# Performance work log

Hardware: AMD Instinct MI355X
Metric: run time of the kernel (lower is better)

Reference implementation:

```python
import jax, jax.numpy as jnp
import numpy as np

NUM_HEADS = 16

def setup_inputs() -> dict:
    key = jax.random.key(0)
    ks = jax.random.split(key, 8)
    T, S, B, E = 2048, 2048, 4, 1024
    s = 0.02
    return {
        "query": jax.random.normal(ks[0], (T, B, E), jnp.float32),
        "key": jax.random.normal(ks[1], (S, B, E), jnp.float32),
        "value": jax.random.normal(ks[2], (S, B, E), jnp.float32),
        "q_proj_weight": jax.random.normal(ks[3], (E, E), jnp.float32) * s,
        "k_proj_weight": jax.random.normal(ks[4], (E, E), jnp.float32) * s,
        "v_proj_weight": jax.random.normal(ks[5], (E, E), jnp.float32) * s,
        "out_proj_weight": jax.random.normal(ks[6], (E, E), jnp.float32) * s,
        "out_proj_bias": jax.random.normal(ks[7], (E,), jnp.float32) * s,
    }

def reference(query, key, value, q_proj_weight, k_proj_weight, v_proj_weight,
              out_proj_weight, out_proj_bias):
    T, B, E = query.shape
    S = key.shape[0]
    H = NUM_HEADS
    hd = E // H
    # F.linear: x @ W.T
    q = jnp.einsum('tbe,fe->tbf', query, q_proj_weight) * (float(hd) ** -0.5)
    k = jnp.einsum('sbe,fe->sbf', key, k_proj_weight)
    v = jnp.einsum('sbe,fe->sbf', value, v_proj_weight)
    # [len, B, E] -> [B*H, len, hd]  (view then transpose, as in torch)
    q = q.reshape(T, B * H, hd).transpose(1, 0, 2)
    k = k.reshape(S, B * H, hd).transpose(1, 0, 2)
    v = v.reshape(S, B * H, hd).transpose(1, 0, 2)
    scores = jnp.einsum('nth,nsh->nts', q, k)      # [B*H, T, S]
    attn = jax.nn.softmax(scores, axis=-1)          # dropout p=0.0 -> identity
    out = jnp.einsum('nts,nsh->nth', attn, v)       # [B*H, T, hd]
    out = out.transpose(1, 0, 2).reshape(T, B, E)
    attn_output = jnp.einsum('tbe,fe->tbf', out, out_proj_weight) + out_proj_bias
    # faithful to original: view(num_heads, batch, T, S) of the [B*H,T,S] buffer
    avg_weights = attn.reshape(H, B, T, S).sum(axis=0) / H  # [B, T, S]
    return attn_output, avg_weights
```

## Files before the change

kernel.cpp:

```cpp
#include <hip/hip_runtime.h>
#include <stdint.h>

#define T_LEN 2048
#define S_LEN 2048
#define BATCH 4
#define EMB 1024
#define NH 16
#define HD 64
#define MROWS 8192

typedef __attribute__((ext_vector_type(8))) __bf16 bfx8;
typedef __attribute__((ext_vector_type(4))) float fx4;
typedef __attribute__((ext_vector_type(16))) float fx16;
typedef __attribute__((ext_vector_type(8))) unsigned short usx8;
typedef __attribute__((ext_vector_type(2))) unsigned int ux2;
typedef __attribute__((ext_vector_type(4))) unsigned int ux4;

typedef __attribute__((address_space(1))) const void GV;
typedef __attribute__((address_space(3))) void LV;
#define GLL(gp, lp) __builtin_amdgcn_global_load_lds((GV*)(gp), (LV*)(lp), 16, 0, 0)

#define QSCALE 0.18033688011112042591f
#define M0F 12.0f

static __device__ __forceinline__ unsigned short f2bf(float f) {
  unsigned int u = __float_as_uint(f);
  u += 0x7fffu + ((u >> 16) & 1u);
  return (unsigned short)(u >> 16);
}

static __device__ __forceinline__ unsigned int cvt_pk(float lo, float hi) {
  unsigned int r;
  asm("v_cvt_pk_bf16_f32 %0, %1, %2" : "=v"(r) : "v"(lo), "v"(hi));
  return r;
}

static __device__ __forceinline__ void plswap(unsigned int &a, unsigned int &b) {
  auto r = __builtin_amdgcn_permlane32_swap((int)a, (int)b, false, false);
  a = (unsigned int)r[0];
  b = (unsigned int)r[1];
}

#define PIPE_BARRIER(N)                                              \
  do {                                                               \
    asm volatile("s_waitcnt vmcnt(" #N ")" ::: "memory");            \
    __builtin_amdgcn_s_barrier();                                    \
    asm volatile("" ::: "memory");                                   \
  } while (0)

__global__ __launch_bounds__(256) void cast_all(
    const float* __restrict__ q, const float* __restrict__ k, const float* __restrict__ v,
    const float* __restrict__ wq, const float* __restrict__ wk, const float* __restrict__ wv,
    const float* __restrict__ wo,
    unsigned short* __restrict__ xq, unsigned short* __restrict__ xk, unsigned short* __restrict__ xv,
    unsigned short* __restrict__ bwq, unsigned short* __restrict__ bwk, unsigned short* __restrict__ bwv,
    unsigned short* __restrict__ bwo)
{
  const long IN8 = (long)MROWS * EMB / 8;
  const long W8  = (long)EMB * EMB / 8;
  const long total = 3 * IN8 + 4 * W8;
  for (long i = (long)blockIdx.x * 256 + threadIdx.x; i < total; i += (long)gridDim.x * 256) {
    const float* s; unsigned short* d; long off;
    if (i < 3 * IN8) {
      long wch = i / IN8; off = i - wch * IN8;
      s = (wch == 0) ? q : (wch == 1) ? k : v;
      d = (wch == 0) ? xq : (wch == 1) ? xk : xv;
    } else {
      long j = i - 3 * IN8; long wch = j / W8; off = j - wch * W8;
      s = (wch == 0) ? wq : (wch == 1) ? wk : (wch == 2) ? wv : wo;
      d = (wch == 0) ? bwq : (wch == 1) ? bwk : (wch == 2) ? bwv : bwo;
    }
    const float4* sp = (const float4*)(s + off * 8);
    float4 a = sp[0], b2 = sp[1];
    usx8 r;
    r[0] = f2bf(a.x);  r[1] = f2bf(a.y);  r[2] = f2bf(a.z);  r[3] = f2bf(a.w);
    r[4] = f2bf(b2.x); r[5] = f2bf(b2.y); r[6] = f2bf(b2.z); r[7] = f2bf(b2.w);
    *(usx8*)(d + off * 8) = r;
  }
}

template<int EPI>
__global__ __launch_bounds__(256) void gemm_bt(
    const unsigned short* __restrict__ A,
    const unsigned short* __restrict__ Bw,
    void* __restrict__ Cp,
    const float* __restrict__ bias,
    float scale)
{
  __shared__ unsigned short As[3][128 * 32];
  __shared__ unsigned short Bs[3][128 * 32];
  const int tid = threadIdx.x;
  const int lane = tid & 63;
  const int w = tid >> 6, wr = w >> 1, wc = w & 1;
  const int lr = lane & 15, lhi = lane >> 4;
  const long rowA0 = (long)blockIdx.x * 128;
  const long rowB0 = (long)blockIdx.y * 128;
  fx4 acc[4][4] = {};

  auto stage = [&](int kt, int bf) {
#pragma unroll
    for (int i = 0; i < 2; ++i) {
      int c = tid + i * 256;
      int r = c >> 2, ci = c & 3;
      int cs = ci ^ ((r >> 1) & 3);
      GLL(A + (rowA0 + r) * 1024 + kt * 32 + cs * 8, &As[bf][c * 8]);
      GLL(Bw + (rowB0 + r) * 1024 + kt * 32 + cs * 8, &Bs[bf][c * 8]);
    }
  };

  stage(0, 0);
  stage(1, 1);
  for (int kt = 0; kt < 32; ++kt) {
    const int bf = kt % 3;
    if (kt < 31) PIPE_BARRIER(4); else PIPE_BARRIER(0);
    if (kt + 2 < 32) stage(kt + 2, (kt + 2) % 3);
    bfx8 af[4], bwf[4];
#pragma unroll
    for (int m = 0; m < 4; ++m) {
      int r = wr * 64 + m * 16 + lr;
      af[m] = *(const bfx8*)&As[bf][r * 32 + ((lhi ^ ((r >> 1) & 3)) * 8)];
    }
#pragma unroll
    for (int n = 0; n < 4; ++n) {
      int r = wc * 64 + n * 16 + lr;
      bwf[n] = *(const bfx8*)&Bs[bf][r * 32 + ((lhi ^ ((r >> 1) & 3)) * 8)];
    }
    __builtin_amdgcn_s_setprio(1);
#pragma unroll
    for (int m = 0; m < 4; ++m)
#pragma unroll
      for (int n = 0; n < 4; ++n)
        acc[m][n] = __builtin_amdgcn_mfma_f32_16x16x32_bf16(af[m], bwf[n], acc[m][n], 0, 0, 0);
    __builtin_amdgcn_s_setprio(0);
  }
  if (EPI == 0) {
    unsigned short* out = (unsigned short*)Cp;
#pragma unroll
    for (int m = 0; m < 4; ++m)
#pragma unroll
      for (int n = 0; n < 4; ++n)
#pragma unroll
        for (int j = 0; j < 4; ++j) {
          long row = rowA0 + wr * 64 + m * 16 + lhi * 4 + j;
          long col = rowB0 + wc * 64 + n * 16 + lr;
          long t = row >> 2, b = row & 3;
          long h = col >> 6, d = col & 63;
          out[((b * 16 + h) * 2048 + t) * 64 + d] = f2bf(acc[m][n][j] * scale);
        }
  } else if (EPI == 1) {
    float* out = (float*)Cp;
#pragma unroll
    for (int m = 0; m < 4; ++m)
#pragma unroll
      for (int n = 0; n < 4; ++n)
#pragma unroll
        for (int j = 0; j < 4; ++j) {
          long row = rowA0 + wr * 64 + m * 16 + lhi * 4 + j;
          long col = rowB0 + wc * 64 + n * 16 + lr;
          out[row * 1024 + col] = acc[m][n][j] + bias[col];
        }
  } else {
    unsigned short* out = (unsigned short*)Cp;
#pragma unroll
    for (int m = 0; m < 4; ++m)
#pragma unroll
      for (int n = 0; n < 4; ++n)
#pragma unroll
        for (int j = 0; j < 4; ++j) {
          long row = rowA0 + wr * 64 + m * 16 + lhi * 4 + j;
          long col = rowB0 + wc * 64 + n * 16 + lr;
          long s = row >> 2, b = row & 3;
          long h = col >> 6, d = col & 63;
          out[(((b * 16 + h) * 64 + d) << 11) + s] = f2bf(acc[m][n][j]);
        }
  }
}

__global__ __launch_bounds__(512, 4) void flash_fwd(
    const unsigned short* __restrict__ qs, const unsigned short* __restrict__ ks,
    const unsigned short* __restrict__ vt, unsigned short* __restrict__ os,
    float* __restrict__ lgi)
{
  __shared__ unsigned short Kl[3][64 * 64];
  __shared__ unsigned short Vl[3][64 * 64];
  const int tid = threadIdx.x;
  const int w = tid >> 6;
  const int lane = tid & 63;
  const int l31 = lane & 31;
  const int hi = lane >> 5;
  const long bh = blockIdx.x;
  const long t0 = (long)blockIdx.y * 256;
  const unsigned short* kb0 = ks + bh * 2048 * 64;
  const unsigned short* vb0 = vt + bh * 64 * 2048;

  bfx8 qf[4];
  {
    const unsigned short* qp = qs + (bh * 2048 + t0 + w * 32 + l31) * 64;
#pragma unroll
    for (int ksl = 0; ksl < 4; ++ksl)
      qf[ksl] = *(const bfx8*)(qp + ksl * 16 + hi * 8);
  }

  bfx8 ones8;
  {
    union { ux4 u; bfx8 b; } ou;
    ou.u.x = ou.u.y = ou.u.z = ou.u.w = 0x3F803F80u;
    ones8 = ou.b;
  }

  fx16 oacc[2] = {};
  fx16 lacc = {};

  auto stage = [&](int st, int bf) {
    const unsigned short* kp = kb0 + st * 64 * 64;
    const unsigned short* vp = vb0 + st * 64;
    int r = tid >> 3, pc = tid & 7;
    int cs = pc ^ (r & 7);
    GLL(kp + r * 64 + cs * 8, &Kl[bf][tid * 8]);
    GLL(vp + (long)r * 2048 + cs * 8, &Vl[bf][tid * 8]);
  };

  stage(0, 0);
  stage(1, 1);
  for (int st = 0; st < 32; ++st) {
    const int bf = st % 3;
    if (st < 31) PIPE_BARRIER(2); else PIPE_BARRIER(0);
    if (st + 2 < 32) stage(st + 2, (st + 2) % 3);
    fx16 sc[2] = {};
    __builtin_amdgcn_s_setprio(1);
#pragma unroll
    for (int ksl = 0; ksl < 4; ++ksl)
#pragma unroll
      for (int kb = 0; kb < 2; ++kb) {
        int row = kb * 32 + l31;
        int phys = (2 * ksl + hi) ^ (row & 7);
        bfx8 af = *(const bfx8*)&Kl[bf][row * 64 + phys * 8];
        sc[kb] = __builtin_amdgcn_mfma_f32_32x32x16_bf16(af, qf[ksl], sc[kb], 0, 0, 0);
      }
    __builtin_amdgcn_s_setprio(0);
#pragma unroll
    for (int kb = 0; kb < 2; ++kb)
#pragma unroll
      for (int r = 0; r < 16; ++r)
        sc[kb][r] = __builtin_amdgcn_exp2f(sc[kb][r] - M0F);
#pragma unroll
    for (int ksl = 0; ksl < 4; ++ksl) {
      const int kb = ksl >> 1;
      const int tb = 2 * (ksl & 1);
      unsigned int A0 = cvt_pk(sc[kb][tb * 4 + 0], sc[kb][tb * 4 + 1]);
      unsigned int A1 = cvt_pk(sc[kb][tb * 4 + 2], sc[kb][tb * 4 + 3]);
      unsigned int B0 = cvt_pk(sc[kb][tb * 4 + 4], sc[kb][tb * 4 + 5]);
      unsigned int B1 = cvt_pk(sc[kb][tb * 4 + 6], sc[kb][tb * 4 + 7]);
      plswap(A0, B0);
      plswap(A1, B1);
      ux4 uw; uw.x = A0; uw.y = A1; uw.z = B0; uw.w = B1;
      union { ux4 u; bfx8 b; } cvv; cvv.u = uw;
      bfx8 pa = cvv.b;
      __builtin_amdgcn_s_setprio(1);
#pragma unroll
      for (int db = 0; db < 2; ++db) {
        int row = db * 32 + l31;
        int phys = (2 * ksl + hi) ^ (row & 7);
        bfx8 vf = *(const bfx8*)&Vl[bf][row * 64 + phys * 8];
        oacc[db] = __builtin_amdgcn_mfma_f32_32x32x16_bf16(vf, pa, oacc[db], 0, 0, 0);
      }
      lacc = __builtin_amdgcn_mfma_f32_32x32x16_bf16(ones8, pa, lacc, 0, 0, 0);
      __builtin_amdgcn_s_setprio(0);
    }
  }
  const long b_ = bh >> 4, h_ = bh & 15;
  {
    float li = 1.f / lacc[0];
    long t = t0 + w * 32 + l31;
    unsigned short* ob = os + (t * 4 + b_) * 1024 + h_ * 64;
#pragma unroll
    for (int db = 0; db < 2; ++db)
#pragma unroll
      for (int tt = 0; tt < 4; ++tt) {
        int d0i = db * 32 + tt * 8 + hi * 4;
        unsigned int u0 = cvt_pk(oacc[db][tt * 4 + 0] * li, oacc[db][tt * 4 + 1] * li);
        unsigned int u1 = cvt_pk(oacc[db][tt * 4 + 2] * li, oacc[db][tt * 4 + 3] * li);
        ux2 uu; uu.x = u0; uu.y = u1;
        *(ux2*)(ob + d0i) = uu;
      }
    if (hi == 0) lgi[bh * 2048 + t] = li;
  }
}

__global__ __launch_bounds__(256) void avg_kernel(
    const unsigned short* __restrict__ qs, const unsigned short* __restrict__ ks,
    const float* __restrict__ lgi, float* __restrict__ avg)
{
  __shared__ unsigned short Qs[3][64 * 64];
  __shared__ unsigned short Ks[3][128 * 64];
  __shared__ float lgl[16 * 64];
  const int tid = threadIdx.x, lane = tid & 63, w = tid >> 6;
  const int lr = lane & 15, g = lane >> 4;
  const long b = blockIdx.z;
  const long t0 = (long)blockIdx.x * 64;
  const long s0 = (long)blockIdx.y * 128;
  fx4 aacc[8] = {};
  const int qr = w * 16 + lr;

  auto stage = [&](int h, int bf) {
    long bh = b * 16 + h;
    const unsigned short* qb = qs + (bh * 2048 + t0) * 64;
    const unsigned short* kb = ks + (bh * 2048 + s0) * 64;
#pragma unroll
    for (int i = 0; i < 2; ++i) {
      int c = tid + i * 256, r = c >> 3, cs = (c & 7) ^ (r & 7);
      GLL(qb + r * 64 + cs * 8, &Qs[bf][c * 8]);
    }
#pragma unroll
    for (int i = 0; i < 4; ++i) {
      int c = tid + i * 256, r = c >> 3, cs = (c & 7) ^ (r & 7);
      GLL(kb + r * 64 + cs * 8, &Ks[bf][c * 8]);
    }
  };

  GLL(&lgi[(b * 16 + (tid >> 4)) * 2048 + t0 + (tid & 15) * 4], &lgl[tid * 4]);
  stage(0, 0);
  stage(1, 1);
  for (int h = 0; h < 16; ++h) {
    const int bf = h % 3;
    if (h < 15) PIPE_BARRIER(6); else PIPE_BARRIER(0);
    if (h + 2 < 16) stage(h + 2, (h + 2) % 3);
    fx4 sacc[8] = {};
    __builtin_amdgcn_s_setprio(1);
#pragma unroll
    for (int k2 = 0; k2 < 2; ++k2) {
      bfx8 aq = *(const bfx8*)&Qs[bf][qr * 64 + (((k2 * 4 + g) ^ (qr & 7)) * 8)];
#pragma unroll
      for (int n = 0; n < 8; ++n) {
        int kr = n * 16 + lr;
        bfx8 bk = *(const bfx8*)&Ks[bf][kr * 64 + (((k2 * 4 + g) ^ (kr & 7)) * 8)];
        sacc[n] = __builtin_amdgcn_mfma_f32_16x16x32_bf16(aq, bk, sacc[n], 0, 0, 0);
      }
    }
    __builtin_amdgcn_s_setprio(0);
#pragma unroll
    for (int j = 0; j < 4; ++j) {
      float lj = lgl[h * 64 + w * 16 + g * 4 + j];
#pragma unroll
      for (int n = 0; n < 8; ++n)
        aacc[n][j] += __builtin_amdgcn_exp2f(sacc[n][j] - M0F) * lj;
    }
  }
#pragma unroll
  for (int j = 0; j < 4; ++j) {
    long t = t0 + w * 16 + g * 4 + j;
#pragma unroll
    for (int n = 0; n < 8; ++n)
      avg[(b * 2048 + t) * 2048 + s0 + n * 16 + lr] = aacc[n][j] * 0.0625f;
  }
}

extern "C" void kernel_launch(void* const* d_in, const int* in_sizes, int n_in,
                              void* d_out, int out_size, void* d_ws, size_t ws_size,
                              hipStream_t stream)
{
  const float* q   = (const float*)d_in[0];
  const float* k   = (const float*)d_in[1];
  const float* v   = (const float*)d_in[2];
  const float* wq  = (const float*)d_in[3];
  const float* wk  = (const float*)d_in[4];
  const float* wv  = (const float*)d_in[5];
  const float* wo  = (const float*)d_in[6];
  const float* bias= (const float*)d_in[7];
  char* ws = (char*)d_ws;
  const long MB = 1024 * 1024;
  unsigned short* bwq = (unsigned short*)(ws + 0 * MB);
  unsigned short* bwk = (unsigned short*)(ws + 2 * MB);
  unsigned short* bwv = (unsigned short*)(ws + 4 * MB);
  unsigned short* bwo = (unsigned short*)(ws + 6 * MB);
  unsigned short* xq  = (unsigned short*)(ws + 8 * MB);
  unsigned short* xk  = (unsigned short*)(ws + 24 * MB);
  unsigned short* xv  = (unsigned short*)(ws + 40 * MB);
  unsigned short* qsb = (unsigned short*)(ws + 56 * MB);
  unsigned short* ksb = (unsigned short*)(ws + 72 * MB);
  unsigned short* vtb = (unsigned short*)(ws + 104 * MB);
  unsigned short* osb = (unsigned short*)(ws + 120 * MB);
  float* lgi = (float*)(ws + 137 * MB);
  float* outp = (float*)d_out;

  cast_all<<<14336, 256, 0, stream>>>(q, k, v, wq, wk, wv, wo,
                                      xq, xk, xv, bwq, bwk, bwv, bwo);
  dim3 gg(64, 8);
  gemm_bt<0><<<gg, 256, 0, stream>>>(xq, bwq, qsb, nullptr, QSCALE);
  gemm_bt<0><<<gg, 256, 0, stream>>>(xk, bwk, ksb, nullptr, 1.0f);
  gemm_bt<2><<<gg, 256, 0, stream>>>(xv, bwv, vtb, nullptr, 1.0f);
  flash_fwd<<<dim3(64, 8), 512, 0, stream>>>(qsb, ksb, vtb, osb, lgi);
  avg_kernel<<<dim3(32, 16, 4), 256, 0, stream>>>(qsb, ksb, lgi, outp + 8388608);
  gemm_bt<1><<<gg, 256, 0, stream>>>(osb, bwo, d_out, bias, 1.0f);
}
```

Baseline: 320.1 us.

## Enlarge avg_kernel tile to 128x128 with 32x32 MFMA and double buffering

Reworks the averaged-attention-weights kernel so each block computes a 128x128 tile of scores using 32x32x16 bf16 MFMAs instead of a 64x128 tile with 16x16x32 ones. It halves the grid and switches from a triple-buffered pipeline with partial barriers to a double buffer with a full __syncthreads each head. The goal is more reuse per K-tile load and fewer total Q/K reloads, at the cost of larger per-thread accumulators and a less overlapped load schedule.

```diff
diff --git a/kernel.cpp b/kernel.cpp
--- a/kernel.cpp
+++ b/kernel.cpp
@@ -287,71 +287,72 @@
   }
 }
 
-__global__ __launch_bounds__(256) void avg_kernel(
+__global__ __launch_bounds__(256, 2) void avg_kernel(
     const unsigned short* __restrict__ qs, const unsigned short* __restrict__ ks,
     const float* __restrict__ lgi, float* __restrict__ avg)
 {
-  __shared__ unsigned short Qs[3][64 * 64];
-  __shared__ unsigned short Ks[3][128 * 64];
-  __shared__ float lgl[16 * 64];
+  __shared__ unsigned short Qs[2][128 * 64];
+  __shared__ unsigned short Ks[2][128 * 64];
+  __shared__ float lgl[16 * 128];
   const int tid = threadIdx.x, lane = tid & 63, w = tid >> 6;
-  const int lr = lane & 15, g = lane >> 4;
+  const int l31 = lane & 31, hi = lane >> 5;
   const long b = blockIdx.z;
-  const long t0 = (long)blockIdx.x * 64;
+  const long t0 = (long)blockIdx.x * 128;
   const long s0 = (long)blockIdx.y * 128;
-  fx4 aacc[8] = {};
-  const int qr = w * 16 + lr;
+  fx16 aacc[4] = {};
 
   auto stage = [&](int h, int bf) {
     long bh = b * 16 + h;
     const unsigned short* qb = qs + (bh * 2048 + t0) * 64;
     const unsigned short* kb = ks + (bh * 2048 + s0) * 64;
 #pragma unroll
-    for (int i = 0; i < 2; ++i) {
+    for (int i = 0; i < 4; ++i) {
       int c = tid + i * 256, r = c >> 3, cs = (c & 7) ^ (r & 7);
       GLL(qb + r * 64 + cs * 8, &Qs[bf][c * 8]);
-    }
-#pragma unroll
-    for (int i = 0; i < 4; ++i) {
-      int c = tid + i * 256, r = c >> 3, cs = (c & 7) ^ (r & 7);
       GLL(kb + r * 64 + cs * 8, &Ks[bf][c * 8]);
     }
   };
 
-  GLL(&lgi[(b * 16 + (tid >> 4)) * 2048 + t0 + (tid & 15) * 4], &lgl[tid * 4]);
+#pragma unroll
+  for (int i = 0; i < 2; ++i) {
+    int c = tid + i * 256;
+    GLL(&lgi[(b * 16 + (c >> 5)) * 2048 + t0 + (c & 31) * 4], &lgl[c * 4]);
+  }
   stage(0, 0);
-  stage(1, 1);
+  __syncthreads();
+  int buf = 0;
   for (int h = 0; h < 16; ++h) {
-    const int bf = h % 3;
-    if (h < 15) PIPE_BARRIER(6); else PIPE_BARRIER(0);
-    if (h + 2 < 16) stage(h + 2, (h + 2) % 3);
-    fx4 sacc[8] = {};
+    if (h < 15) stage(h + 1, buf ^ 1);
+    fx16 sacc[4] = {};
+    const int arow = w * 32 + l31;
     __builtin_amdgcn_s_setprio(1);
 #pragma unroll
-    for (int k2 = 0; k2 < 2; ++k2) {
-      bfx8 aq = *(const bfx8*)&Qs[bf][qr * 64 + (((k2 * 4 + g) ^ (qr & 7)) * 8)];
-#pragma unroll
-      for (int n = 0; n < 8; ++n) {
-        int kr = n * 16 + lr;
-        bfx8 bk = *(const bfx8*)&Ks[bf][kr * 64 + (((k2 * 4 + g) ^ (kr & 7)) * 8)];
-        sacc[n] = __builtin_amdgcn_mfma_f32_16x16x32_bf16(aq, bk, sacc[n], 0, 0, 0);
+    for (int ksl = 0; ksl < 4; ++ksl) {
+      bfx8 aq = *(const bfx8*)&Qs[buf][arow * 64 + (((2 * ksl + hi) ^ (arow & 7)) * 8)];
+#pragma unroll
+      for (int n = 0; n < 4; ++n) {
+        int brow = n * 32 + l31;
+        bfx8 bk = *(const bfx8*)&Ks[buf][brow * 64 + (((2 * ksl + hi) ^ (brow & 7)) * 8)];
+        sacc[n] = __builtin_amdgcn_mfma_f32_32x32x16_bf16(aq, bk, sacc[n], 0, 0, 0);
       }
     }
     __builtin_amdgcn_s_setprio(0);
 #pragma unroll
-    for (int j = 0; j < 4; ++j) {
-      float lj = lgl[h * 64 + w * 16 + g * 4 + j];
-#pragma unroll
-      for (int n = 0; n < 8; ++n)
-        aacc[n][j] += __builtin_amdgcn_exp2f(sacc[n][j] - M0F) * lj;
-    }
-  }
-#pragma unroll
-  for (int j = 0; j < 4; ++j) {
-    long t = t0 + w * 16 + g * 4 + j;
-#pragma unroll
-    for (int n = 0; n < 8; ++n)
-      avg[(b * 2048 + t) * 2048 + s0 + n * 16 + lr] = aacc[n][j] * 0.0625f;
+    for (int r = 0; r < 16; ++r) {
+      float lj = lgl[h * 128 + w * 32 + (r & 3) + 8 * (r >> 2) + 4 * hi];
+#pragma unroll
+      for (int n = 0; n < 4; ++n)
+        aacc[n][r] += __builtin_amdgcn_exp2f(sacc[n][r] - M0F) * lj;
+    }
+    __syncthreads();
+    buf ^= 1;
+  }
+#pragma unroll
+  for (int r = 0; r < 16; ++r) {
+    long t = t0 + w * 32 + (r & 3) + 8 * (r >> 2) + 4 * hi;
+#pragma unroll
+    for (int n = 0; n < 4; ++n)
+      avg[(b * 2048 + t) * 2048 + s0 + n * 32 + l31] = aacc[n][r] * 0.0625f;
   }
 }
 
@@ -390,6 +391,6 @@
   gemm_bt<0><<<gg, 256, 0, stream>>>(xk, bwk, ksb, nullptr, 1.0f);
   gemm_bt<2><<<gg, 256, 0, stream>>>(xv, bwv, vtb, nullptr, 1.0f);
   flash_fwd<<<dim3(64, 8), 512, 0, stream>>>(qsb, ksb, vtb, osb, lgi);
-  avg_kernel<<<dim3(32, 16, 4), 256, 0, stream>>>(qsb, ksb, lgi, outp + 8388608);
+  avg_kernel<<<dim3(16, 16, 4), 256, 0, stream>>>(qsb, ksb, lgi, outp + 8388608);
   gemm_bt<1><<<gg, 256, 0, stream>>>(osb, bwo, d_out, bias, 1.0f);
 }
```

After: 300.8 us. 1.06x faster.
